# Performance work log

Hardware: AMD Instinct MI355X
Metric: run time of the kernel (lower is better)

Reference implementation:

```python
import jax, jax.numpy as jnp
import numpy as np

D_FEAT = 6
HID = 256
T = 60
B_DAYS = 4
STOCKS = 512
TRAIN_DAYS = 240
K_DAY = 10
N_NEIGHBOR = 10
SLOPE = 0.01  # nn.LeakyReLU default


def setup_inputs() -> dict:
    key = jax.random.key(0)
    ks = jax.random.split(key, 32)
    g = lambda i, shape, s=0.05: (jax.random.normal(ks[i], shape, dtype=jnp.float32) * s)
    inp = jax.random.normal(ks[0], (B_DAYS, STOCKS, D_FEAT * T), dtype=jnp.float32)
    train_hidden = jax.random.normal(ks[1], (TRAIN_DAYS, STOCKS, HID), dtype=jnp.float32)
    train_hidden_day = jax.random.normal(ks[2], (TRAIN_DAYS, HID), dtype=jnp.float32)
    return {
        "inp": inp,
        "train_hidden": train_hidden,
        "train_hidden_day": train_hidden_day,
        # GRU layer 0 (input D_FEAT) and layer 1 (input HID); gates [r,z,n] stacked -> 3*HID
        "W_ih0": g(3, (3 * HID, D_FEAT)), "W_hh0": g(4, (3 * HID, HID)),
        "b_ih0": g(5, (3 * HID,)), "b_hh0": g(6, (3 * HID,)),
        "W_ih1": g(7, (3 * HID, HID)), "W_hh1": g(8, (3 * HID, HID)),
        "b_ih1": g(9, (3 * HID,)), "b_hh1": g(10, (3 * HID,)),
        # lins MLP 256->512->512->256
        "lin0_W": g(11, (512, HID)), "lin0_b": g(12, (512,)),
        "lin1_W": g(13, (512, 512)), "lin1_b": g(14, (512,)),
        "lin2_W": g(15, (HID, 512)), "lin2_b": g(16, (HID,)),
        # projections (no bias) and output head
        "proj1_W": g(17, (HID, HID)), "proj2_W": g(18, (HID, HID)),
        "fc_W": g(19, (1, 2 * HID)), "fc_b": g(20, (1,)),
    }


def _leaky(x):
    return jnp.where(x >= 0, x, SLOPE * x)


def _gru_layer(x, W_ih, W_hh, b_ih, b_hh):
    # x: [N, T, in] -> [N, T, HID]
    xW = jnp.einsum('nti,gi->ntg', x, W_ih) + b_ih  # precompute input gates
    def step(h, xw):
        gh = h @ W_hh.T + b_hh
        xr, xz, xn = jnp.split(xw, 3, axis=-1)
        hr, hz, hn = jnp.split(gh, 3, axis=-1)
        r = jax.nn.sigmoid(xr + hr)
        z = jax.nn.sigmoid(xz + hz)
        n = jnp.tanh(xn + r * hn)
        h = (1.0 - z) * n + z * h
        return h, h
    h0 = jnp.zeros((x.shape[0], W_hh.shape[1]), x.dtype)
    _, hs = jax.lax.scan(step, h0, jnp.swapaxes(xW, 0, 1))
    return jnp.swapaxes(hs, 0, 1)


def _cos_sim(x, y):
    xy = x @ y.T
    xn = jnp.sqrt(jnp.sum(x * x, axis=1))[:, None]
    yn = jnp.sqrt(jnp.sum(y * y, axis=1))[:, None]
    cs = xy / (xn @ yn.T)
    return jnp.where(jnp.isnan(cs), 0.0, cs)


def reference(inp, train_hidden, train_hidden_day,
              W_ih0, W_hh0, b_ih0, b_hh0, W_ih1, W_hh1, b_ih1, b_hh1,
              lin0_W, lin0_b, lin1_W, lin1_b, lin2_W, lin2_b,
              proj1_W, proj2_W, fc_W, fc_b):
    B, S = inp.shape[0], inp.shape[1]
    x = inp.reshape(B * S, D_FEAT, -1).transpose(0, 2, 1)  # [N, T, d_feat]
    h = _gru_layer(x, W_ih0, W_hh0, b_ih0, b_hh0)
    h = _gru_layer(h, W_ih1, W_hh1, b_ih1, b_hh1)
    out = h[:, -1, :]                                      # [N, HID]
    mb = _leaky(out @ lin0_W.T + lin0_b)
    mb = _leaky(mb @ lin1_W.T + lin1_b)
    mb = _leaky(mb @ lin2_W.T + lin2_b)                    # mini_batch_out [N, HID]
    mb_day = jnp.mean(mb.reshape(B, S, -1), axis=1)        # [B, HID]
    day_sim = _cos_sim(mb_day, train_hidden_day)           # [B, TRAIN_DAYS]
    _, day_idx = jax.lax.top_k(day_sim, K_DAY)             # [B, K_DAY]
    sample = train_hidden[day_idx].reshape(-1, train_hidden.shape[-1])  # [B*K_DAY*S, HID]
    q = mb @ proj1_W.T
    kh = sample @ proj2_W.T
    cs = _cos_sim(q, kh)                                   # [N, B*K_DAY*S]
    vals, idx = jax.lax.top_k(cs, N_NEIGHBOR)              # per-row top-k (distinct cols)
    # sparse mask (ones/n_neighbor) * cos_sim, then sparse @ kh == weighted gather-sum
    agg = jnp.einsum('nk,nkh->nh', vals / N_NEIGHBOR, kh[idx])
    cat = jnp.concatenate([mb, agg], axis=1)               # [N, 2*HID]
    y = (cat @ fc_W.T + fc_b).squeeze(-1)
    return y.reshape(B, -1)
```

## Files before the change

### kernel.cpp

```cpp
#include <hip/hip_runtime.h>
#include <cmath>
#include <cstdint>

#define D_FEAT 6
#define T_SEQ  60
#define HID    256
#define G3     768
#define NROW   2048
#define NSAMP  20480

__device__ __forceinline__ float sigmoidf_(float x) { return 1.0f / (1.0f + expf(-x)); }

struct PrepArgs {
  const float* src[9];
  float* dst[9];
  int N[9], K[9], ro[9], pk[9];
};

__global__ void prep_weights(PrepArgs a) {
  int seg = blockIdx.y;
  const float* S = a.src[seg];
  float* D = a.dst[seg];
  int N = a.N[seg], K = a.K[seg], ro = a.ro[seg], pk = a.pk[seg];
  int total = N * K;
  for (int i = blockIdx.x * blockDim.x + threadIdx.x; i < total; i += gridDim.x * blockDim.x) {
    int n = i / K, k = i - n * K;
    if (pk) {
      int u = n >> 8, cn = n & 255;
      int kg = k + ro;
      D[(size_t)((kg >> 2) * 3 + u) * 1024 + cn * 4 + (kg & 3)] = S[i];
    } else {
      D[(size_t)(k + ro) * N + n] = S[i];
    }
  }
}

#define FMA8(alo, ahi, b, accrow) \
  accrow[0] += alo.x * (b); accrow[1] += alo.y * (b); accrow[2] += alo.z * (b); accrow[3] += alo.w * (b); \
  accrow[4] += ahi.x * (b); accrow[5] += ahi.y * (b); accrow[6] += ahi.z * (b); accrow[7] += ahi.w * (b);

__device__ __forceinline__ void kloop64(const float* __restrict__ A,
                                        const float* __restrict__ B,
                                        float (&acc)[3][8])
{
  float Bc[3][4], Bn[3][4];
#pragma unroll
  for (int u = 0; u < 3; ++u)
    *(float4*)Bc[u] = *(const float4*)(B + u * 1024);
#pragma unroll 4
  for (int k4 = 0; k4 < 16; ++k4) {
    const float* p = B + (size_t)((k4 + 1) & 15) * 3072;
#pragma unroll
    for (int u = 0; u < 3; ++u)
      *(float4*)Bn[u] = *(const float4*)(p + u * 1024);
#pragma unroll
    for (int c = 0; c < 4; ++c) {
      float4 alo = *(const float4*)(A + (k4 * 4 + c) * 8);
      float4 ahi = *(const float4*)(A + (k4 * 4 + c) * 8 + 4);
      FMA8(alo, ahi, Bc[0][c], acc[0]);
      FMA8(alo, ahi, Bc[1][c], acc[1]);
      FMA8(alo, ahi, Bc[2][c], acc[2]);
    }
#pragma unroll
    for (int u = 0; u < 3; ++u)
#pragma unroll
      for (int c = 0; c < 4; ++c) Bc[u][c] = Bn[u][c];
  }
}

__global__ __attribute__((amdgpu_flat_work_group_size(1024, 1024), amdgpu_waves_per_eu(4, 4)))
void gru_fused(const float* __restrict__ inp, const float* __restrict__ Whh0p,
               const float* __restrict__ Wcatp, const float* __restrict__ WTih0,
               const float* __restrict__ bih0, const float* __restrict__ bhh0,
               const float* __restrict__ bih1, const float* __restrict__ bhh1,
               float* __restrict__ hrow)
{
  __shared__ float h0A[2048], h0B[2048];
  __shared__ float h1A[2048], h1B[2048];
  __shared__ float xls[2880];
  __shared__ float exch[256 * 97];

  const int tid = threadIdx.x;
  const int col = tid & 255;
  const int q   = tid >> 8;
  const int m0  = blockIdx.x * 8;
  const int r0  = q * 2;

  for (int c = tid; c < 2880; c += 1024) {
    int row = c / 360, it = c - row * 360;
    xls[it * 8 + row] = inp[(size_t)(m0 + row) * 360 + it];
  }
  for (int c = tid; c < 2048; c += 1024) { h0A[c] = 0.f; h1A[c] = 0.f; }

  float h0c[2] = {0.f, 0.f}, h1c[2] = {0.f, 0.f};

  float b_ih0[3], b_hh0[3], b_ih1[3], b_hh1[3];
#pragma unroll
  for (int u = 0; u < 3; ++u) {
    int o = u * 256 + col;
    b_ih0[u] = bih0[o]; b_hh0[u] = bhh0[o];
    b_ih1[u] = bih1[o]; b_hh1[u] = bhh1[o];
  }
  __syncthreads();

  const int aoff = q << 9;
  const float* Bhh = Whh0p + (size_t)(q * 16) * 3072 + col * 4;
  const float* Bc0 = Wcatp + (size_t)(q * 16) * 3072 + col * 4;
  const float* Bc1 = Wcatp + (size_t)(64 + q * 16) * 3072 + col * 4;
  float* exc = exch + col * 97;

  for (int t = 0; t < T_SEQ; ++t) {
    const float* h0cur = (t & 1) ? h0B : h0A;
    float*       h0nxt = (t & 1) ? h0A : h0B;
    const float* h1cur = (t & 1) ? h1B : h1A;
    float*       h1nxt = (t & 1) ? h1A : h1B;

    float gh[3][8];
#pragma unroll
    for (int u = 0; u < 3; ++u)
#pragma unroll
      for (int r = 0; r < 8; ++r) gh[u][r] = 0.f;
    kloop64(h0cur + aoff, Bhh, gh);

    float xw[2][3];
#pragma unroll
    for (int r2 = 0; r2 < 2; ++r2)
#pragma unroll
      for (int u = 0; u < 3; ++u) xw[r2][u] = b_ih0[u];
#pragma unroll
    for (int i = 0; i < 6; ++i) {
      float x0 = xls[(i * 60 + t) * 8 + r0];
      float x1 = xls[(i * 60 + t) * 8 + r0 + 1];
#pragma unroll
      for (int u = 0; u < 3; ++u) {
        float b = WTih0[i * G3 + u * 256 + col];
        xw[0][u] += x0 * b;
        xw[1][u] += x1 * b;
      }
    }
#pragma unroll
    for (int p = 0; p < 4; ++p) {
      if (p == q) continue;
      int qrel = (q < p) ? q : q - 1;
#pragma unroll
      for (int u = 0; u < 3; ++u) {
        exc[((p * 3 + qrel) * 3 + u) * 2 + 0] = gh[u][p * 2 + 0];
        exc[((p * 3 + qrel) * 3 + u) * 2 + 1] = gh[u][p * 2 + 1];
      }
    }
    __syncthreads();
    {
      float g[3][2];
#pragma unroll
      for (int u = 0; u < 3; ++u) { g[u][0] = gh[u][r0]; g[u][1] = gh[u][r0 + 1]; }
#pragma unroll
      for (int qs = 0; qs < 3; ++qs)
#pragma unroll
        for (int u = 0; u < 3; ++u) {
          g[u][0] += exc[((q * 3 + qs) * 3 + u) * 2 + 0];
          g[u][1] += exc[((q * 3 + qs) * 3 + u) * 2 + 1];
        }
#pragma unroll
      for (int r2 = 0; r2 < 2; ++r2) {
        float rr = sigmoidf_(xw[r2][0] + (g[0][r2] + b_hh0[0]));
        float zz = sigmoidf_(xw[r2][1] + (g[1][r2] + b_hh0[1]));
        float nn = tanhf(xw[r2][2] + rr * (g[2][r2] + b_hh0[2]));
        h0c[r2] = (1.f - zz) * nn + zz * h0c[r2];
        h0nxt[col * 8 + r0 + r2] = h0c[r2];
      }
    }
    __syncthreads();

    float acc[3][8];
#pragma unroll
    for (int u = 0; u < 3; ++u)
#pragma unroll
      for (int r = 0; r < 8; ++r) acc[u][r] = 0.f;
    kloop64(h0nxt + aoff, Bc0, acc);
    float xn8[8];
#pragma unroll
    for (int r = 0; r < 8; ++r) { xn8[r] = acc[2][r]; acc[2][r] = 0.f; }
    kloop64(h1cur + aoff, Bc1, acc);

#pragma unroll
    for (int p = 0; p < 4; ++p) {
      if (p == q) continue;
      int qrel = (q < p) ? q : q - 1;
      int base = (p * 3 + qrel) * 8;
#pragma unroll
      for (int r2 = 0; r2 < 2; ++r2) {
        exc[base + 0 + r2] = acc[0][p * 2 + r2];
        exc[base + 2 + r2] = acc[1][p * 2 + r2];
        exc[base + 4 + r2] = xn8[p * 2 + r2];
        exc[base + 6 + r2] = acc[2][p * 2 + r2];
      }
    }
    __syncthreads();
    {
      float R[2], Z[2], XN[2], HN[2];
#pragma unroll
      for (int r2 = 0; r2 < 2; ++r2) {
        R[r2] = acc[0][r0 + r2]; Z[r2] = acc[1][r0 + r2];
        XN[r2] = xn8[r0 + r2];   HN[r2] = acc[2][r0 + r2];
      }
#pragma unroll
      for (int qs = 0; qs < 3; ++qs) {
        int base = (q * 3 + qs) * 8;
#pragma unroll
        for (int r2 = 0; r2 < 2; ++r2) {
          R[r2]  += exc[base + 0 + r2];
          Z[r2]  += exc[base + 2 + r2];
          XN[r2] += exc[base + 4 + r2];
          HN[r2] += exc[base + 6 + r2];
        }
      }
#pragma unroll
      for (int r2 = 0; r2 < 2; ++r2) {
        float rr = sigmoidf_((R[r2] + b_ih1[0]) + b_hh1[0]);
        float zz = sigmoidf_((Z[r2] + b_ih1[1]) + b_hh1[1]);
        float nn = tanhf((XN[r2] + b_ih1[2]) + rr * (HN[r2] + b_hh1[2]));
        h1c[r2] = (1.f - zz) * nn + zz * h1c[r2];
        h1nxt[col * 8 + r0 + r2] = h1c[r2];
      }
    }
    __syncthreads();
  }

#pragma unroll
  for (int r2 = 0; r2 < 2; ++r2)
    hrow[(size_t)(m0 + r0 + r2) * 256 + col] = h1c[r2];
}

__global__ __launch_bounds__(256, 2)
void gemm_act(const float* __restrict__ A, const int* __restrict__ rowsrc,
              const float* __restrict__ WT, const float* __restrict__ bias,
              float* __restrict__ C, int M, int N, int K, int act)
{
  __shared__ float4 As4[128 * 32];
  const int tx = threadIdx.x, ty = threadIdx.y;
  const int tid = ty * 32 + tx;
  const int n0 = blockIdx.x * 32, m0 = blockIdx.y * 32;
  const int K4 = K >> 2;

  for (int c = tid; c < K4 * 32; c += 256) {
    int k4 = c % K4, m = c / K4;
    int row = m0 + m;
    if (rowsrc) row = rowsrc[row];
    As4[k4 * 32 + m] = *(const float4*)(A + (size_t)row * K + k4 * 4);
  }
  __syncthreads();

  float acc[4] = {0,0,0,0};
  const int n = n0 + tx;
  const float* pb = WT + n;

  float bc[4], bn_[4];
#pragma unroll
  for (int kk = 0; kk < 4; ++kk) bc[kk] = pb[(size_t)kk * N];
  for (int k4 = 0; k4 < K4; ++k4) {
    int nk4 = (k4 + 1 < K4) ? (k4 + 1) : 0;
    const float* pn = pb + (size_t)nk4 * 4 * N;
#pragma unroll
    for (int kk = 0; kk < 4; ++kk) bn_[kk] = pn[(size_t)kk * N];
    float4 a0 = As4[k4 * 32 + ty * 4 + 0];
    float4 a1 = As4[k4 * 32 + ty * 4 + 1];
    float4 a2 = As4[k4 * 32 + ty * 4 + 2];
    float4 a3 = As4[k4 * 32 + ty * 4 + 3];
#pragma unroll
    for (int kk = 0; kk < 4; ++kk) {
      float b = bc[kk];
      acc[0] += ((const float*)&a0)[kk] * b;
      acc[1] += ((const float*)&a1)[kk] * b;
      acc[2] += ((const float*)&a2)[kk] * b;
      acc[3] += ((const float*)&a3)[kk] * b;
    }
#pragma unroll
    for (int qq = 0; qq < 4; ++qq) bc[qq] = bn_[qq];
  }
  float bb = bias ? bias[n] : 0.f;
#pragma unroll
  for (int r = 0; r < 4; ++r) {
    float v = acc[r] + bb;
    if (act) v = (v >= 0.f) ? v : 0.01f * v;
    C[(size_t)(m0 + ty * 4 + r) * N + n] = v;
  }
}

__global__ void mbday_part(const float* __restrict__ mbf, float* __restrict__ part) {
  int d = blockIdx.x, sl = blockIdx.y, c = threadIdx.x;
  float s = 0.f;
  int base = d * 512 + sl * 64;
  for (int st = 0; st < 64; ++st) s += mbf[(size_t)(base + st) * 256 + c];
  part[(size_t)(d * 8 + sl) * 256 + c] = s;
}

__global__ void mbday_fin(const float* __restrict__ part, float* __restrict__ mbday) {
  int d = blockIdx.x, c = threadIdx.x;
  float s = 0.f;
#pragma unroll
  for (int p = 0; p < 8; ++p) s += part[(size_t)(d * 8 + p) * 256 + c];
  mbday[d * 256 + c] = s * (1.0f / 512.0f);
}

__global__ void daytopk_kernel(const float* __restrict__ mbday, const float* __restrict__ thd,
                               int* __restrict__ dayidx) {
  __shared__ float mbs[256];
  __shared__ float sim[256];
  __shared__ float red[256];
  __shared__ int   redi[256];
  const int d = blockIdx.x, t = threadIdx.x;
  mbs[t] = mbday[d * 256 + t];
  __syncthreads();
  red[t] = mbs[t] * mbs[t];
  __syncthreads();
  for (int o = 128; o; o >>= 1) { if (t < o) red[t] += red[t + o]; __syncthreads(); }
  float xn = sqrtf(red[0]);
  float v = -INFINITY;
  if (t < 240) {
    float dot = 0.f, yn2 = 0.f;
    for (int k = 0; k < 256; ++k) {
      float y = thd[t * 256 + k];
      dot += mbs[k] * y;
      yn2 += y * y;
    }
    float den = xn * sqrtf(yn2);
    v = (den > 0.f) ? dot / den : 0.f;
  }
  sim[t] = v;
  __syncthreads();
  for (int it = 0; it < 10; ++it) {
    red[t] = sim[t]; redi[t] = t;
    __syncthreads();
    for (int o = 128; o; o >>= 1) {
      if (t < o) {
        if (red[t + o] > red[t] || (red[t + o] == red[t] && redi[t + o] < redi[t])) {
          red[t] = red[t + o]; redi[t] = redi[t + o];
        }
      }
      __syncthreads();
    }
    if (t == 0) { int bi = redi[0]; dayidx[d * 10 + it] = bi; sim[bi] = -INFINITY; }
    __syncthreads();
  }
}

__global__ void rowsrc_kernel(const int* __restrict__ dayidx, int* __restrict__ rowsrc) {
  int r = blockIdx.x * 256 + threadIdx.x;
  if (r < NSAMP) rowsrc[r] = dayidx[r >> 9] * 512 + (r & 511);
}

__global__ void rownorm_kernel(const float* __restrict__ X, float* __restrict__ out, int rows) {
  int w = threadIdx.x >> 6;
  int lane = threadIdx.x & 63;
  int row = blockIdx.x * 4 + w;
  if (row >= rows) return;
  float4 x = *(const float4*)(X + (size_t)row * 256 + lane * 4);
  float s = x.x * x.x + x.y * x.y + x.z * x.z + x.w * x.w;
#pragma unroll
  for (int o = 32; o; o >>= 1) s += __shfl_down(s, o, 64);
  if (lane == 0) out[row] = sqrtf(s);
}

__global__ void qnorm_kernel(float* __restrict__ q, const float* __restrict__ qn) {
  int i = blockIdx.x * 256 + threadIdx.x;
  int row = i >> 8;
  float n = qn[row];
  q[i] = (n > 0.f) ? q[i] / n : 0.f;
}

__global__ void khT_kernel(const float* __restrict__ kh, const float* __restrict__ khn,
                           float* __restrict__ khT) {
  __shared__ float tile[32][33];
  int jb = blockIdx.x * 32;
  int kb = blockIdx.y * 32;
  int tx = threadIdx.x & 31, tyy = threadIdx.x >> 5;
  for (int rr = tyy; rr < 32; rr += 8) {
    float n = khn[jb + rr];
    float v = kh[(size_t)(jb + rr) * 256 + kb + tx];
    tile[rr][tx] = (n > 0.f) ? v / n : 0.f;
  }
  __syncthreads();
  for (int rr = tyy; rr < 32; rr += 8) {
    khT[(size_t)(kb + rr) * NSAMP + jb + tx] = tile[tx][rr];
  }
}

__global__ __launch_bounds__(256, 4)
void csmax_kernel(const float* __restrict__ qh, const float* __restrict__ khT,
                  float* __restrict__ topvp, int* __restrict__ topip)
{
  __shared__ float4 qs[256][2];
  __shared__ float csch[8 * 512];
  const int tid = threadIdx.x;
  const int split = blockIdx.x & 7;
  const int m0 = (blockIdx.x >> 3) * 8;
  {
    int k = tid;
    float4 v0, v1;
    v0.x = qh[(size_t)(m0 + 0) * 256 + k]; v0.y = qh[(size_t)(m0 + 1) * 256 + k];
    v0.z = qh[(size_t)(m0 + 2) * 256 + k]; v0.w = qh[(size_t)(m0 + 3) * 256 + k];
    v1.x = qh[(size_t)(m0 + 4) * 256 + k]; v1.y = qh[(size_t)(m0 + 5) * 256 + k];
    v1.z = qh[(size_t)(m0 + 6) * 256 + k]; v1.w = qh[(size_t)(m0 + 7) * 256 + k];
    qs[k][0] = v0; qs[k][1] = v1;
  }
  __syncthreads();
  const int lane = tid & 63;
  const int wv = tid >> 6;

  float tv0[10], tv1[10];
  int   tj0[10], tj1[10];
  int   tn0 = 0, tn1 = 0;
  float tmv0 = -INFINITY, tmv1 = -INFINITY;
  int   tmi0 = 0, tmi1 = 0;

  auto process_row = [&](int r, float (&tv)[10], int (&tj)[10], int& tn,
                         float& tmv, int& tmi, int jb) {
    float4 c0 = *(const float4*)&csch[r * 512 + lane * 8];
    float4 c1 = *(const float4*)&csch[r * 512 + lane * 8 + 4];
    float cv[8] = {c0.x, c0.y, c0.z, c0.w, c1.x, c1.y, c1.z, c1.w};
    const int cj0 = jb + lane * 8;
    while (true) {
      float bv = -INFINITY; int bj = 0x7fffffff;
#pragma unroll
      for (int u = 0; u < 8; ++u) {
        if (cv[u] > bv) { bv = cv[u]; bj = cj0 + u; }
      }
#pragma unroll
      for (int o = 32; o; o >>= 1) {
        float ov = __shfl_down(bv, o, 64);
        int   oj = __shfl_down(bj, o, 64);
        if (ov > bv || (ov == bv && oj < bj)) { bv = ov; bj = oj; }
      }
      bv = __shfl(bv, 0, 64); bj = __shfl(bj, 0, 64);
      bool take;
      if (tn < 10) take = true;
      else take = (bv > tmv) || (bv == tmv && bj < tmi);
      if (!take) break;
      if (tn < 10) {
#pragma unroll
        for (int s = 0; s < 10; ++s) if (s == tn) { tv[s] = bv; tj[s] = bj; }
        tn++;
        if (tn == 10) {
          float mv = tv[0]; int mi = tj[0];
#pragma unroll
          for (int s = 1; s < 10; ++s) {
            bool w = (tv[s] < mv) || (tv[s] == mv && tj[s] > mi);
            if (w) { mv = tv[s]; mi = tj[s]; }
          }
          tmv = mv; tmi = mi;
        }
      } else {
        int ms = 0; float mv = tv[0]; int mi = tj[0];
#pragma unroll
        for (int s = 1; s < 10; ++s) {
          bool w = (tv[s] < mv) || (tv[s] == mv && tj[s] > mi);
          if (w) { ms = s; mv = tv[s]; mi = tj[s]; }
        }
#pragma unroll
        for (int s = 0; s < 10; ++s) if (s == ms) { tv[s] = bv; tj[s] = bj; }
        mv = tv[0]; mi = tj[0];
#pragma unroll
        for (int s = 1; s < 10; ++s) {
          bool w = (tv[s] < mv) || (tv[s] == mv && tj[s] > mi);
          if (w) { mv = tv[s]; mi = tj[s]; }
        }
        tmv = mv; tmi = mi;
      }
#pragma unroll
      for (int u = 0; u < 8; ++u) if (cj0 + u == bj) cv[u] = -INFINITY;
    }
  };

  for (int ci = 0; ci < 5; ++ci) {
    const int ch = split * 5 + ci;
    const int jb = ch * 512;
    float acc[8][2];
#pragma unroll
    for (int r = 0; r < 8; ++r) { acc[r][0] = 0.f; acc[r][1] = 0.f; }
    const float* kp = khT + jb + tid;

    float b0c[4], b1c[4], b0n[4], b1n[4];
#pragma unroll
    for (int kk = 0; kk < 4; ++kk) {
      b0c[kk] = kp[(size_t)kk * NSAMP];
      b1c[kk] = kp[(size_t)kk * NSAMP + 256];
    }
    for (int k4 = 0; k4 < 64; ++k4) {
      int nk4 = (k4 + 1) & 63;
      const float* pn = kp + (size_t)nk4 * 4 * NSAMP;
#pragma unroll
      for (int kk = 0; kk < 4; ++kk) {
        b0n[kk] = pn[(size_t)kk * NSAMP];
        b1n[kk] = pn[(size_t)kk * NSAMP + 256];
      }
#pragma unroll
      for (int kk = 0; kk < 4; ++kk) {
        float4 qa = qs[k4 * 4 + kk][0];
        float4 qb = qs[k4 * 4 + kk][1];
        float b0 = b0c[kk], b1 = b1c[kk];
        acc[0][0] += qa.x * b0; acc[1][0] += qa.y * b0; acc[2][0] += qa.z * b0; acc[3][0] += qa.w * b0;
        acc[4][0] += qb.x * b0; acc[5][0] += qb.y * b0; acc[6][0] += qb.z * b0; acc[7][0] += qb.w * b0;
        acc[0][1] += qa.x * b1; acc[1][1] += qa.y * b1; acc[2][1] += qa.z * b1; acc[3][1] += qa.w * b1;
        acc[4][1] += qb.x * b1; acc[5][1] += qb.y * b1; acc[6][1] += qb.z * b1; acc[7][1] += qb.w * b1;
      }
#pragma unroll
      for (int qq = 0; qq < 4; ++qq) { b0c[qq] = b0n[qq]; b1c[qq] = b1n[qq]; }
    }
    __syncthreads();
#pragma unroll
    for (int r = 0; r < 8; ++r) {
      csch[r * 512 + tid] = acc[r][0];
      csch[r * 512 + 256 + tid] = acc[r][1];
    }
    __syncthreads();
    process_row(wv,     tv0, tj0, tn0, tmv0, tmi0, jb);
    process_row(wv + 4, tv1, tj1, tn1, tmv1, tmi1, jb);
  }
  __syncthreads();

  if (lane == 0) {
    int row0 = m0 + wv;
#pragma unroll
    for (int s = 0; s < 10; ++s) {
      topvp[(size_t)row0 * 80 + split * 10 + s] = tv0[s];
      topip[(size_t)row0 * 80 + split * 10 + s] = tj0[s];
    }
    int row1 = m0 + wv + 4;
#pragma unroll
    for (int s = 0; s < 10; ++s) {
      topvp[(size_t)row1 * 80 + split * 10 + s] = tv1[s];
      topip[(size_t)row1 * 80 + split * 10 + s] = tj1[s];
    }
  }
}

__global__ void merge_topk(const float* __restrict__ topvp, const int* __restrict__ topip,
                           float* __restrict__ topv, int* __restrict__ topi)
{
  const int wv = threadIdx.x >> 6;
  const int lane = threadIdx.x & 63;
  const int row = blockIdx.x * 4 + wv;
  float v0 = topvp[(size_t)row * 80 + lane];
  int   i0 = topip[(size_t)row * 80 + lane];
  float v1 = (lane < 16) ? topvp[(size_t)row * 80 + 64 + lane] : -INFINITY;
  int   i1 = (lane < 16) ? topip[(size_t)row * 80 + 64 + lane] : 0x7fffffff;
  for (int s = 0; s < 10; ++s) {
    float bv = v0; int bj = i0;
    if (v1 > bv || (v1 == bv && i1 < bj)) { bv = v1; bj = i1; }
#pragma unroll
    for (int o = 1; o < 64; o <<= 1) {
      float ov = __shfl_xor(bv, o, 64);
      int   oj = __shfl_xor(bj, o, 64);
      if (ov > bv || (ov == bv && oj < bj)) { bv = ov; bj = oj; }
    }
    if (lane == 0) { topv[row * 10 + s] = bv; topi[row * 10 + s] = bj; }
    if (i0 == bj) { v0 = -INFINITY; i0 = 0x7fffffff; }
    if (i1 == bj) { v1 = -INFINITY; i1 = 0x7fffffff; }
  }
}

__global__ void final_kernel(const float* __restrict__ mb, const float* __restrict__ kh,
                             const float* __restrict__ topv, const int* __restrict__ topi,
                             const float* __restrict__ fcW, const float* __restrict__ fcb,
                             float* __restrict__ y)
{
  __shared__ float red[256];
  int n = blockIdx.x, c = threadIdx.x;
  float agg = 0.f;
#pragma unroll
  for (int k = 0; k < 10; ++k) {
    float w = topv[n * 10 + k] / 10.0f;
    int idx = topi[n * 10 + k];
    agg += w * kh[(size_t)idx * 256 + c];
  }
  float val = fcW[c] * mb[(size_t)n * 256 + c] + fcW[256 + c] * agg;
  red[c] = val;
  __syncthreads();
  for (int o = 128; o; o >>= 1) { if (c < o) red[c] += red[c + o]; __syncthreads(); }
  if (c == 0) y[n] = red[0] + fcb[0];
}

extern "C" void kernel_launch(void* const* d_in, const int* in_sizes, int n_in,
                              void* d_out, int out_size, void* d_ws, size_t ws_size,
                              hipStream_t stream)
{
  const float* inp    = (const float*)d_in[0];
  const float* trainh = (const float*)d_in[1];
  const float* thd    = (const float*)d_in[2];
  const float* Wih0   = (const float*)d_in[3];
  const float* Whh0   = (const float*)d_in[4];
  const float* bih0   = (const float*)d_in[5];
  const float* bhh0   = (const float*)d_in[6];
  const float* Wih1   = (const float*)d_in[7];
  const float* Whh1   = (const float*)d_in[8];
  const float* bih1   = (const float*)d_in[9];
  const float* bhh1   = (const float*)d_in[10];
  const float* lin0W  = (const float*)d_in[11];
  const float* lin0b  = (const float*)d_in[12];
  const float* lin1W  = (const float*)d_in[13];
  const float* lin1b  = (const float*)d_in[14];
  const float* lin2W  = (const float*)d_in[15];
  const float* lin2b  = (const float*)d_in[16];
  const float* p1W    = (const float*)d_in[17];
  const float* p2W    = (const float*)d_in[18];
  const float* fcW    = (const float*)d_in[19];
  const float* fcb    = (const float*)d_in[20];

  float* ws = (float*)d_ws;
  float* WT_hh0 = ws + 0;
  float* WTcat  = ws + 196608;
  float* WT_l0  = ws + 589824;
  float* WT_l1  = ws + 720896;
  float* WT_l2  = ws + 983040;
  float* WT_p1  = ws + 1114112;
  float* WT_p2  = ws + 1179648;
  float* hrow   = ws + 1245184;
  float* mb1    = ws + 3342336;
  float* mb2    = ws + 4390912;
  float* mbf    = ws + 5439488;
  float* mbday  = ws + 5963776;
  float* qbuf   = ws + 5964800;
  float* kh     = ws + 6489088;
  float* khT    = ws + 11731968;
  float* khn    = ws + 16974848;
  float* qn     = ws + 16995328;
  float* topv   = ws + 16997376;
  int*   dayidx = (int*)(ws + 17017856);
  int*   rowsrc = (int*)(ws + 17017920);
  int*   topi   = (int*)(ws + 17038400);
  float* topvp  = mb1;
  int*   topip  = (int*)(mb1 + 163840);
  float* WT_ih0 = mb2;
  float* mbpart = mb2;

  PrepArgs pa;
  pa.src[0] = Whh0;  pa.dst[0] = WT_hh0; pa.N[0] = 768; pa.K[0] = 256; pa.ro[0] = 0;   pa.pk[0] = 1;
  pa.src[1] = Wih1;  pa.dst[1] = WTcat;  pa.N[1] = 768; pa.K[1] = 256; pa.ro[1] = 0;   pa.pk[1] = 1;
  pa.src[2] = Whh1;  pa.dst[2] = WTcat;  pa.N[2] = 768; pa.K[2] = 256; pa.ro[2] = 256; pa.pk[2] = 1;
  pa.src[3] = lin0W; pa.dst[3] = WT_l0;  pa.N[3] = 512; pa.K[3] = 256; pa.ro[3] = 0;   pa.pk[3] = 0;
  pa.src[4] = lin1W; pa.dst[4] = WT_l1;  pa.N[4] = 512; pa.K[4] = 512; pa.ro[4] = 0;   pa.pk[4] = 0;
  pa.src[5] = lin2W; pa.dst[5] = WT_l2;  pa.N[5] = 256; pa.K[5] = 512; pa.ro[5] = 0;   pa.pk[5] = 0;
  pa.src[6] = p1W;   pa.dst[6] = WT_p1;  pa.N[6] = 256; pa.K[6] = 256; pa.ro[6] = 0;   pa.pk[6] = 0;
  pa.src[7] = p2W;   pa.dst[7] = WT_p2;  pa.N[7] = 256; pa.K[7] = 256; pa.ro[7] = 0;   pa.pk[7] = 0;
  pa.src[8] = Wih0;  pa.dst[8] = WT_ih0; pa.N[8] = 768; pa.K[8] = 6;   pa.ro[8] = 0;   pa.pk[8] = 0;
  prep_weights<<<dim3(64, 9), dim3(256), 0, stream>>>(pa);

  gru_fused<<<256, 1024, 0, stream>>>(inp, WT_hh0, WTcat, WT_ih0, bih0, bhh0, bih1, bhh1, hrow);

  gemm_act<<<dim3(16, 64), dim3(32, 8), 0, stream>>>(hrow, nullptr, WT_l0, lin0b, mb1, 2048, 512, 256, 1);
  gemm_act<<<dim3(16, 64), dim3(32, 8), 0, stream>>>(mb1, nullptr, WT_l1, lin1b, mb2, 2048, 512, 512, 1);
  gemm_act<<<dim3(8, 64),  dim3(32, 8), 0, stream>>>(mb2, nullptr, WT_l2, lin2b, mbf, 2048, 256, 512, 1);

  mbday_part<<<dim3(4, 8), 256, 0, stream>>>(mbf, mbpart);
  mbday_fin<<<4, 256, 0, stream>>>(mbpart, mbday);
  daytopk_kernel<<<4, 256, 0, stream>>>(mbday, thd, dayidx);
  rowsrc_kernel<<<80, 256, 0, stream>>>(dayidx, rowsrc);

  gemm_act<<<dim3(8, 640), dim3(32, 8), 0, stream>>>(trainh, rowsrc, WT_p2, nullptr, kh, 20480, 256, 256, 0);
  gemm_act<<<dim3(8, 64),  dim3(32, 8), 0, stream>>>(mbf, nullptr, WT_p1, nullptr, qbuf, 2048, 256, 256, 0);

  rownorm_kernel<<<5120, 256, 0, stream>>>(kh, khn, 20480);
  rownorm_kernel<<<512, 256, 0, stream>>>(qbuf, qn, 2048);
  qnorm_kernel<<<2048, 256, 0, stream>>>(qbuf, qn);
  khT_kernel<<<dim3(640, 8), 256, 0, stream>>>(kh, khn, khT);

  csmax_kernel<<<2048, 256, 0, stream>>>(qbuf, khT, topvp, topip);
  merge_topk<<<512, 256, 0, stream>>>(topvp, topip, topv, topi);
  final_kernel<<<2048, 256, 0, stream>>>(mbf, kh, topv, topi, fcW, fcb, (float*)d_out);

  (void)in_sizes; (void)n_in; (void)out_size; (void)ws_size;
}
```

Before: 3.732 ms.

## Reduce GRU split-K partials onto one quarter-group and do gates there

Changes the split-K reduction in the fused GRU recurrence. Previously each of the four thread quarters exchanged partial sums with every other quarter and each computed gates for two rows. Now quarters 1-3 write their full partials to shared memory and quarter 0 reduces all of them and computes the gate nonlinearities for all 8 rows, using vectorized LDS stores. This cuts the number of LDS exchange writes and bank conflicts, but serializes the gate math and input projection onto a quarter of the threads while the other three quarters sit idle.

```diff
diff --git a/kernel.cpp b/kernel.cpp
--- a/kernel.cpp
+++ b/kernel.cpp
@@ -84,7 +84,6 @@
   const int col = tid & 255;
   const int q   = tid >> 8;
   const int m0  = blockIdx.x * 8;
-  const int r0  = q * 2;
 
   for (int c = tid; c < 2880; c += 1024) {
     int row = c / 360, it = c - row * 360;
@@ -92,7 +91,9 @@
   }
   for (int c = tid; c < 2048; c += 1024) { h0A[c] = 0.f; h1A[c] = 0.f; }
 
-  float h0c[2] = {0.f, 0.f}, h1c[2] = {0.f, 0.f};
+  float h0c[8], h1c[8];
+#pragma unroll
+  for (int r = 0; r < 8; ++r) { h0c[r] = 0.f; h1c[r] = 0.f; }
 
   float b_ih0[3], b_hh0[3], b_ih1[3], b_hh1[3];
 #pragma unroll
@@ -107,7 +108,8 @@
   const float* Bhh = Whh0p + (size_t)(q * 16) * 3072 + col * 4;
   const float* Bc0 = Wcatp + (size_t)(q * 16) * 3072 + col * 4;
   const float* Bc1 = Wcatp + (size_t)(64 + q * 16) * 3072 + col * 4;
-  float* exc = exch + col * 97;
+  float* exc  = exch + col * 97;
+  float* excw = exch + col * 97 + (q - 1) * 32;
 
   for (int t = 0; t < T_SEQ; ++t) {
     const float* h0cur = (t & 1) ? h0B : h0A;
@@ -122,52 +124,51 @@
       for (int r = 0; r < 8; ++r) gh[u][r] = 0.f;
     kloop64(h0cur + aoff, Bhh, gh);
 
-    float xw[2][3];
-#pragma unroll
-    for (int r2 = 0; r2 < 2; ++r2)
-#pragma unroll
-      for (int u = 0; u < 3; ++u) xw[r2][u] = b_ih0[u];
-#pragma unroll
-    for (int i = 0; i < 6; ++i) {
-      float x0 = xls[(i * 60 + t) * 8 + r0];
-      float x1 = xls[(i * 60 + t) * 8 + r0 + 1];
-#pragma unroll
-      for (int u = 0; u < 3; ++u) {
-        float b = WTih0[i * G3 + u * 256 + col];
-        xw[0][u] += x0 * b;
-        xw[1][u] += x1 * b;
-      }
-    }
-#pragma unroll
-    for (int p = 0; p < 4; ++p) {
-      if (p == q) continue;
-      int qrel = (q < p) ? q : q - 1;
-#pragma unroll
-      for (int u = 0; u < 3; ++u) {
-        exc[((p * 3 + qrel) * 3 + u) * 2 + 0] = gh[u][p * 2 + 0];
-        exc[((p * 3 + qrel) * 3 + u) * 2 + 1] = gh[u][p * 2 + 1];
-      }
-    }
-    __syncthreads();
-    {
-      float g[3][2];
-#pragma unroll
-      for (int u = 0; u < 3; ++u) { g[u][0] = gh[u][r0]; g[u][1] = gh[u][r0 + 1]; }
-#pragma unroll
-      for (int qs = 0; qs < 3; ++qs)
+    if (q != 0) {
+#pragma unroll
+      for (int u = 0; u < 3; ++u)
+#pragma unroll
+        for (int r = 0; r < 8; ++r) excw[u * 8 + r] = gh[u][r];
+    }
+    __syncthreads();
+
+    if (q == 0) {
+#pragma unroll
+      for (int s = 0; s < 3; ++s)
+#pragma unroll
+        for (int u = 0; u < 3; ++u)
+#pragma unroll
+          for (int r = 0; r < 8; ++r) gh[u][r] += exc[s * 32 + u * 8 + r];
+
+      float xw[3][8];
+#pragma unroll
+      for (int u = 0; u < 3; ++u)
+#pragma unroll
+        for (int r = 0; r < 8; ++r) xw[u][r] = b_ih0[u];
+#pragma unroll
+      for (int i = 0; i < 6; ++i) {
+        float4 xlo = *(const float4*)&xls[(i * 60 + t) * 8];
+        float4 xhi = *(const float4*)&xls[(i * 60 + t) * 8 + 4];
 #pragma unroll
         for (int u = 0; u < 3; ++u) {
-          g[u][0] += exc[((q * 3 + qs) * 3 + u) * 2 + 0];
-          g[u][1] += exc[((q * 3 + qs) * 3 + u) * 2 + 1];
+          float b = WTih0[i * G3 + u * 256 + col];
+          xw[u][0] += xlo.x * b; xw[u][1] += xlo.y * b;
+          xw[u][2] += xlo.z * b; xw[u][3] += xlo.w * b;
+          xw[u][4] += xhi.x * b; xw[u][5] += xhi.y * b;
+          xw[u][6] += xhi.z * b; xw[u][7] += xhi.w * b;
         }
-#pragma unroll
-      for (int r2 = 0; r2 < 2; ++r2) {
-        float rr = sigmoidf_(xw[r2][0] + (g[0][r2] + b_hh0[0]));
-        float zz = sigmoidf_(xw[r2][1] + (g[1][r2] + b_hh0[1]));
-        float nn = tanhf(xw[r2][2] + rr * (g[2][r2] + b_hh0[2]));
-        h0c[r2] = (1.f - zz) * nn + zz * h0c[r2];
-        h0nxt[col * 8 + r0 + r2] = h0c[r2];
-      }
+      }
+      float hn[8];
+#pragma unroll
+      for (int r = 0; r < 8; ++r) {
+        float rr = sigmoidf_(xw[0][r] + (gh[0][r] + b_hh0[0]));
+        float zz = sigmoidf_(xw[1][r] + (gh[1][r] + b_hh0[1]));
+        float nn = tanhf(xw[2][r] + rr * (gh[2][r] + b_hh0[2]));
+        h0c[r] = (1.f - zz) * nn + zz * h0c[r];
+        hn[r] = h0c[r];
+      }
+      *(float4*)&h0nxt[col * 8]     = *(float4*)&hn[0];
+      *(float4*)&h0nxt[col * 8 + 4] = *(float4*)&hn[4];
     }
     __syncthreads();
 
@@ -182,53 +183,47 @@
     for (int r = 0; r < 8; ++r) { xn8[r] = acc[2][r]; acc[2][r] = 0.f; }
     kloop64(h1cur + aoff, Bc1, acc);
 
-#pragma unroll
-    for (int p = 0; p < 4; ++p) {
-      if (p == q) continue;
-      int qrel = (q < p) ? q : q - 1;
-      int base = (p * 3 + qrel) * 8;
-#pragma unroll
-      for (int r2 = 0; r2 < 2; ++r2) {
-        exc[base + 0 + r2] = acc[0][p * 2 + r2];
-        exc[base + 2 + r2] = acc[1][p * 2 + r2];
-        exc[base + 4 + r2] = xn8[p * 2 + r2];
-        exc[base + 6 + r2] = acc[2][p * 2 + r2];
-      }
-    }
-    __syncthreads();
-    {
-      float R[2], Z[2], XN[2], HN[2];
-#pragma unroll
-      for (int r2 = 0; r2 < 2; ++r2) {
-        R[r2] = acc[0][r0 + r2]; Z[r2] = acc[1][r0 + r2];
-        XN[r2] = xn8[r0 + r2];   HN[r2] = acc[2][r0 + r2];
-      }
-#pragma unroll
-      for (int qs = 0; qs < 3; ++qs) {
-        int base = (q * 3 + qs) * 8;
-#pragma unroll
-        for (int r2 = 0; r2 < 2; ++r2) {
-          R[r2]  += exc[base + 0 + r2];
-          Z[r2]  += exc[base + 2 + r2];
-          XN[r2] += exc[base + 4 + r2];
-          HN[r2] += exc[base + 6 + r2];
+    if (q != 0) {
+#pragma unroll
+      for (int r = 0; r < 8; ++r) {
+        excw[r]      = acc[0][r];
+        excw[8 + r]  = acc[1][r];
+        excw[16 + r] = xn8[r];
+        excw[24 + r] = acc[2][r];
+      }
+    }
+    __syncthreads();
+
+    if (q == 0) {
+#pragma unroll
+      for (int s = 0; s < 3; ++s)
+#pragma unroll
+        for (int r = 0; r < 8; ++r) {
+          acc[0][r] += exc[s * 32 + r];
+          acc[1][r] += exc[s * 32 + 8 + r];
+          xn8[r]    += exc[s * 32 + 16 + r];
+          acc[2][r] += exc[s * 32 + 24 + r];
         }
-      }
-#pragma unroll
-      for (int r2 = 0; r2 < 2; ++r2) {
-        float rr = sigmoidf_((R[r2] + b_ih1[0]) + b_hh1[0]);
-        float zz = sigmoidf_((Z[r2] + b_ih1[1]) + b_hh1[1]);
-        float nn = tanhf((XN[r2] + b_ih1[2]) + rr * (HN[r2] + b_hh1[2]));
-        h1c[r2] = (1.f - zz) * nn + zz * h1c[r2];
-        h1nxt[col * 8 + r0 + r2] = h1c[r2];
-      }
-    }
-    __syncthreads();
-  }
-
-#pragma unroll
-  for (int r2 = 0; r2 < 2; ++r2)
-    hrow[(size_t)(m0 + r0 + r2) * 256 + col] = h1c[r2];
+      float hn[8];
+#pragma unroll
+      for (int r = 0; r < 8; ++r) {
+        float rr = sigmoidf_((acc[0][r] + b_ih1[0]) + b_hh1[0]);
+        float zz = sigmoidf_((acc[1][r] + b_ih1[1]) + b_hh1[1]);
+        float nn = tanhf((xn8[r] + b_ih1[2]) + rr * (acc[2][r] + b_hh1[2]));
+        h1c[r] = (1.f - zz) * nn + zz * h1c[r];
+        hn[r] = h1c[r];
+      }
+      *(float4*)&h1nxt[col * 8]     = *(float4*)&hn[0];
+      *(float4*)&h1nxt[col * 8 + 4] = *(float4*)&hn[4];
+    }
+    __syncthreads();
+  }
+
+  if (q == 0) {
+#pragma unroll
+    for (int r = 0; r < 8; ++r)
+      hrow[(size_t)(m0 + r) * 256 + col] = h1c[r];
+  }
 }
 
 __global__ __launch_bounds__(256, 2)
```

New measurement: 4.407 ms. 1.18x slower.
